# Optimization experiments

Measured on AMD Instinct MI355X. Metric: run time of the kernel, lower is better.

## Reference

```python
import jax, jax.numpy as jnp
import numpy as np

BS, T, NOBJ = 16, 32, 100
GLOVE, GEMB, ADIM, GCN_DIM, H, ASPACE, RES = 300, 64, 10, 512, 512, 6, 512


def setup_inputs() -> dict:
    key = jax.random.key(0)
    ks = jax.random.split(key, 34)
    rn = lambda k, shp, s=0.02: (jax.random.normal(k, shp, jnp.float32) * s)
    inp = {}
    inp["target"] = jax.random.normal(ks[0], (BS, T, GLOVE), jnp.float32)
    inp["input_"] = jax.random.normal(ks[1], (BS, T, RES, 1, 1), jnp.float32)
    inp["action_probs"] = jax.random.uniform(ks[2], (BS, T, ASPACE), jnp.float32)
    # symmetric normalized adjacency (D^-1/2 A D^-1/2), as normalize_adj produces
    A_raw = (jax.random.uniform(ks[3], (NOBJ, NOBJ)) < 0.1).astype(jnp.float32)
    A_raw = ((A_raw + A_raw.T + jnp.eye(NOBJ)) > 0).astype(jnp.float32)
    dinv = 1.0 / jnp.sqrt(jnp.sum(A_raw, axis=1))
    inp["A"] = A_raw * dinv[:, None] * dinv[None, :]
    inp["all_glove"] = jax.random.normal(ks[4], (NOBJ, GLOVE), jnp.float32)
    inp["Wword"] = rn(ks[5], (GEMB, GLOVE)); inp["bword"] = jnp.zeros((GEMB,))
    inp["Wg"] = rn(ks[6], (GEMB, GLOVE)); inp["bg"] = jnp.zeros((GEMB,))
    inp["Wa"] = rn(ks[7], (ADIM, ASPACE)); inp["ba"] = jnp.zeros((ADIM,))
    inp["W0"] = rn(ks[8], (256, RES + GEMB))
    inp["W1"] = rn(ks[9], (256, 256))
    inp["W2"] = rn(ks[10], (1, 256))
    inp["Wfm"] = rn(ks[11], (GCN_DIM, NOBJ)); inp["bfm"] = jnp.zeros((GCN_DIM,))
    fused_in = RES + GEMB + ADIM + GCN_DIM
    inp["Wf"] = rn(ks[12], (H, fused_in)); inp["bf"] = jnp.zeros((H,))
    inp["Wih"] = rn(ks[13], (4 * H, H)); inp["Whh"] = rn(ks[14], (4 * H, H))
    inp["bih"] = jnp.zeros((4 * H,)); inp["bhh"] = jnp.zeros((4 * H,))
    inp["Wa1"] = rn(ks[15], (128, H)); inp["ba1"] = jnp.zeros((128,))
    inp["Wa2"] = rn(ks[16], (ASPACE, 128)); inp["ba2"] = jnp.zeros((ASPACE,))
    inp["Wc1"] = rn(ks[17], (128, H)); inp["bc1"] = jnp.zeros((128,))
    inp["Wc2"] = rn(ks[18], (1, 128)); inp["bc2"] = jnp.zeros((1,))
    return inp


def _forward(target, input_, action_probs, A, all_glove, Wword, bword, Wg, bg,
             Wa, ba, W0, W1, W2, Wfm, bfm, Wf, bf, Wih, Whh, bih, bhh,
             Wa1, ba1, Wa2, ba2, Wc1, bc1, Wc2, bc2):
    bs, t = target.shape[0], target.shape[1]
    B = bs * t
    feats = input_.reshape(B, RES)                      # [B,512] (squeeze 1x1)
    glove_e = jax.nn.relu(target.reshape(B, GLOVE) @ Wg.T + bg)
    act_e = jax.nn.relu(action_probs.reshape(B, ASPACE) @ Wa.T + ba)
    # GCN branch (all_glove is detached in the original)
    word = jax.lax.stop_gradient(all_glove) @ Wword.T + bword   # [N,GEMB]
    N = A.shape[0]
    class_e = jnp.broadcast_to(feats[:, None, :], (B, N, RES))
    x = jnp.concatenate([class_e, jnp.broadcast_to(word[None], (B, N, GEMB))], -1)
    x = jax.nn.relu(jnp.einsum('nm,bmd->bnd', A, x) @ W0.T)     # [B,N,256]
    x = jax.nn.relu(jnp.einsum('nm,bmd->bnd', A, x) @ W1.T)     # [B,N,256]
    x = jax.nn.relu(jnp.einsum('nm,bmd->bnd', A, x) @ W2.T)     # [B,N,1]
    gcn_e = x[..., 0] @ Wfm.T + bfm                             # [B,GCN_DIM]
    fused = jnp.concatenate([feats, glove_e, act_e, gcn_e], -1)
    out = jax.nn.relu(fused @ Wf.T + bf).reshape(bs, t, H)
    # LSTM (torch gate order i,f,g,o), batch_first, zero init state
    h0 = jnp.zeros((bs, H), out.dtype)
    c0 = jnp.zeros((bs, H), out.dtype)
    def step(carry, xt):
        h, c = carry
        g = xt @ Wih.T + h @ Whh.T + bih + bhh
        i, f, gg, o = jnp.split(g, 4, axis=-1)
        c = jax.nn.sigmoid(f) * c + jax.nn.sigmoid(i) * jnp.tanh(gg)
        h = jax.nn.sigmoid(o) * jnp.tanh(c)
        return (h, c), h
    (hT, cT), hs = jax.lax.scan(step, (h0, c0), out.transpose(1, 0, 2))
    sf = hs.transpose(1, 0, 2).reshape(B, H)
    actor = jax.nn.relu(jax.nn.relu(sf @ Wa1.T + ba1) @ Wa2.T + ba2).reshape(bs, t, ASPACE)
    critic = jax.nn.relu(jax.nn.relu(sf @ Wc1.T + bc1) @ Wc2.T + bc2).reshape(bs, t, 1)
    return actor, critic, hT[None], cT[None]


def reference(target, input_, action_probs, A, all_glove, Wword, bword, Wg, bg,
              Wa, ba, W0, W1, W2, Wfm, bfm, Wf, bf, Wih, Whh, bih, bhh,
              Wa1, ba1, Wa2, ba2, Wc1, bc1, Wc2, bc2):
    return _forward(target, input_, action_probs, A, all_glove, Wword, bword,
                    Wg, bg, Wa, ba, W0, W1, W2, Wfm, bfm, Wf, bf, Wih, Whh,
                    bih, bhh, Wa1, ba1, Wa2, ba2, Wc1, bc1, Wc2, bc2)
```

## Files before the change

### kernel.cpp

```cpp
#include <hip/hip_runtime.h>
#include <cmath>

constexpr int BSZ = 16, T = 32, NOBJ = 100;
constexpr int GLOVE = 300, GEMB = 64, ADIM = 10, GCN_DIM = 512, Hh = 512, ASPACE = 6, RES = 512;
constexpr int Bt = BSZ * T;
constexpr int FUSED_IN = RES + GEMB + ADIM + GCN_DIM;
constexpr int FP = 1120;

typedef __attribute__((ext_vector_type(8))) short bf16x8;
typedef __attribute__((ext_vector_type(4))) float f32x4;

__device__ __forceinline__ unsigned short f2bf(float f) {
    unsigned u = __float_as_uint(f);
    return (unsigned short)((u + 0x7FFFu + ((u >> 16) & 1u)) >> 16);
}
__device__ __forceinline__ unsigned pk2(float a, float b) {
    return (unsigned)f2bf(a) | ((unsigned)f2bf(b) << 16);
}
__device__ __forceinline__ float sigf(float x) { return 1.f / (1.f + __expf(-x)); }

template<bool RELU, int OMODE>
__global__ __launch_bounds__(256)
void mgemm(const unsigned short* __restrict__ A, int lda,
           const unsigned short* __restrict__ B, int ldb,
           float* __restrict__ Cf, unsigned short* __restrict__ Cb, int ldc,
           const float* __restrict__ bias, int K)
{
    const int tid = threadIdx.x;
    const int l = tid & 63, wv = tid >> 6;
    const int m0 = blockIdx.y * 64 + wv * 16;
    const int n0 = blockIdx.x * 64;
    const int lr = l & 15, kg = l >> 4;
    const unsigned short* ap = A + (long)(m0 + lr) * lda + kg * 8;
    const unsigned short* bp = B + (long)(n0 + lr) * ldb + kg * 8;
    const int nk = K >> 5;
    f32x4 acc0 = (f32x4){0.f, 0.f, 0.f, 0.f};
    f32x4 acc1 = acc0, acc2 = acc0, acc3 = acc0;
    bf16x8 a_[4], b0_[4], b1_[4], b2_[4], b3_[4];
#pragma unroll
    for (int s = 0; s < 4; ++s) {
        if (s < nk) {
            int k = s * 32;
            a_[s]  = *(const bf16x8*)(ap + k);
            b0_[s] = *(const bf16x8*)(bp + k);
            b1_[s] = *(const bf16x8*)(bp + 16 * ldb + k);
            b2_[s] = *(const bf16x8*)(bp + 32 * ldb + k);
            b3_[s] = *(const bf16x8*)(bp + 48 * ldb + k);
        }
    }
    for (int i = 0; i < nk; i += 4) {
#pragma unroll
        for (int s = 0; s < 4; ++s) {
            if (i + s < nk) {
                acc0 = __builtin_amdgcn_mfma_f32_16x16x32_bf16(a_[s], b0_[s], acc0, 0, 0, 0);
                acc1 = __builtin_amdgcn_mfma_f32_16x16x32_bf16(a_[s], b1_[s], acc1, 0, 0, 0);
                acc2 = __builtin_amdgcn_mfma_f32_16x16x32_bf16(a_[s], b2_[s], acc2, 0, 0, 0);
                acc3 = __builtin_amdgcn_mfma_f32_16x16x32_bf16(a_[s], b3_[s], acc3, 0, 0, 0);
                if (i + s + 4 < nk) {
                    int k = (i + s + 4) * 32;
                    a_[s]  = *(const bf16x8*)(ap + k);
                    b0_[s] = *(const bf16x8*)(bp + k);
                    b1_[s] = *(const bf16x8*)(bp + 16 * ldb + k);
                    b2_[s] = *(const bf16x8*)(bp + 32 * ldb + k);
                    b3_[s] = *(const bf16x8*)(bp + 48 * ldb + k);
                }
            }
        }
    }
    f32x4 av[4] = {acc0, acc1, acc2, acc3};
#pragma unroll
    for (int nf = 0; nf < 4; ++nf) {
        int n = n0 + nf * 16 + lr;
        float bs = bias ? bias[n] : 0.f;
#pragma unroll
        for (int r = 0; r < 4; ++r) {
            float val = av[nf][r] + bs;
            if (RELU) val = fmaxf(val, 0.f);
            long idx = (long)(m0 + kg * 4 + r) * ldc + n;
            if (OMODE == 0) Cf[idx] = val;
            else            Cb[idx] = f2bf(val);
        }
    }
}

template<bool RELU>
__global__ __launch_bounds__(128)
void gemm32(const float* __restrict__ A, int lda,
            const float* __restrict__ B, int ldb,
            float* __restrict__ C, int ldc,
            const float* __restrict__ bias, int M, int N, int K)
{
    __shared__ float As[32][36];
    __shared__ float Bs[32][68];
    const int tid = threadIdx.x;
    const int m0 = blockIdx.y * 32, n0 = blockIdx.x * 64;
    const int mi = tid >> 4, ni = tid & 15;
    float acc[4][4] = {};
    for (int k0 = 0; k0 < K; k0 += 32) {
        __syncthreads();
#pragma unroll
        for (int l = 0; l < 2; ++l) {
            int e = tid + l * 128;
            int row = e >> 3, kq = (e & 7) << 2;
            float4 va = make_float4(0.f, 0.f, 0.f, 0.f);
            if (m0 + row < M && k0 + kq < K)
                va = *(const float4*)&A[(long)(m0 + row) * lda + k0 + kq];
            As[kq + 0][row] = va.x; As[kq + 1][row] = va.y;
            As[kq + 2][row] = va.z; As[kq + 3][row] = va.w;
        }
#pragma unroll
        for (int l = 0; l < 4; ++l) {
            int e = tid + l * 128;
            int row = e >> 3, kq = (e & 7) << 2;
            float4 vb = make_float4(0.f, 0.f, 0.f, 0.f);
            if (n0 + row < N && k0 + kq < K)
                vb = *(const float4*)&B[(long)(n0 + row) * ldb + k0 + kq];
            Bs[kq + 0][row] = vb.x; Bs[kq + 1][row] = vb.y;
            Bs[kq + 2][row] = vb.z; Bs[kq + 3][row] = vb.w;
        }
        __syncthreads();
#pragma unroll
        for (int k = 0; k < 32; ++k) {
            float4 a4 = *(const float4*)&As[k][4 * mi];
            float4 b4 = *(const float4*)&Bs[k][4 * ni];
            acc[0][0] = fmaf(a4.x, b4.x, acc[0][0]); acc[0][1] = fmaf(a4.x, b4.y, acc[0][1]);
            acc[0][2] = fmaf(a4.x, b4.z, acc[0][2]); acc[0][3] = fmaf(a4.x, b4.w, acc[0][3]);
            acc[1][0] = fmaf(a4.y, b4.x, acc[1][0]); acc[1][1] = fmaf(a4.y, b4.y, acc[1][1]);
            acc[1][2] = fmaf(a4.y, b4.z, acc[1][2]); acc[1][3] = fmaf(a4.y, b4.w, acc[1][3]);
            acc[2][0] = fmaf(a4.z, b4.x, acc[2][0]); acc[2][1] = fmaf(a4.z, b4.y, acc[2][1]);
            acc[2][2] = fmaf(a4.z, b4.z, acc[2][2]); acc[2][3] = fmaf(a4.z, b4.w, acc[2][3]);
            acc[3][0] = fmaf(a4.w, b4.x, acc[3][0]); acc[3][1] = fmaf(a4.w, b4.y, acc[3][1]);
            acc[3][2] = fmaf(a4.w, b4.z, acc[3][2]); acc[3][3] = fmaf(a4.w, b4.w, acc[3][3]);
        }
    }
    const int n = n0 + 4 * ni;
    if (n >= N) return;
    float4 bv = make_float4(0.f, 0.f, 0.f, 0.f);
    if (bias) bv = *(const float4*)&bias[n];
#pragma unroll
    for (int r = 0; r < 4; ++r) {
        int m = m0 + 4 * mi + r;
        if (m >= M) continue;
        float4 v;
        v.x = acc[r][0] + bv.x; v.y = acc[r][1] + bv.y;
        v.z = acc[r][2] + bv.z; v.w = acc[r][3] + bv.w;
        if (RELU) {
            v.x = fmaxf(v.x, 0.f); v.y = fmaxf(v.y, 0.f);
            v.z = fmaxf(v.z, 0.f); v.w = fmaxf(v.w, 0.f);
        }
        *(float4*)&C[(long)m * ldc + n] = v;
    }
}

__global__ __launch_bounds__(256)
void x1pack(const float* __restrict__ u, const float* __restrict__ v,
            const float* __restrict__ rowsum, uint4* __restrict__ X1g)
{
    __shared__ float u_lds[256];
    __shared__ float rs_lds[112];
    const int b = blockIdx.x, tid = threadIdx.x;
    u_lds[tid] = u[(long)b * 256 + tid];
    if (tid < 112) rs_lds[tid] = (tid < 100) ? rowsum[tid] : 0.f;
    __syncthreads();
    uint4* outp = X1g + (size_t)b * 3584;
#pragma unroll
    for (int it = 0; it < 14; ++it) {
        int job = it * 256 + tid;
        int l = job & 63;
        int kt = (job >> 6) & 7;
        int mt = job >> 9;
        int n = mt * 16 + (l & 15);
        int k0 = kt * 32 + ((l >> 4) << 3);
        uint4 p = make_uint4(0, 0, 0, 0);
        if (n < 100) {
            float rsn = rs_lds[n];
            float4 u0 = *(const float4*)&u_lds[k0];
            float4 u1 = *(const float4*)&u_lds[k0 + 4];
            const float4* vp = (const float4*)&v[n * 256 + k0];
            float4 v0 = vp[0], v1 = vp[1];
            float x0 = fmaxf(fmaf(rsn, u0.x, v0.x), 0.f), x1 = fmaxf(fmaf(rsn, u0.y, v0.y), 0.f);
            float x2 = fmaxf(fmaf(rsn, u0.z, v0.z), 0.f), x3 = fmaxf(fmaf(rsn, u0.w, v0.w), 0.f);
            float x4 = fmaxf(fmaf(rsn, u1.x, v1.x), 0.f), x5 = fmaxf(fmaf(rsn, u1.y, v1.y), 0.f);
            float x6 = fmaxf(fmaf(rsn, u1.z, v1.z), 0.f), x7 = fmaxf(fmaf(rsn, u1.w, v1.w), 0.f);
            p = make_uint4(pk2(x0, x1), pk2(x2, x3), pk2(x4, x5), pk2(x6, x7));
        }
        outp[job] = p;
    }
}

constexpr int ZLD = 152;

__global__ __launch_bounds__(256, 2)
void gcn_core(const bf16x8* __restrict__ X1g,
              const float* __restrict__ Aglob,
              const bf16x8* __restrict__ W1f,
              const bf16x8* __restrict__ Af,
              const float* __restrict__ w2,
              unsigned short* __restrict__ x3b)
{
    __shared__ unsigned short Z1Ts[128 * ZLD];
    __shared__ float w2l[256];
    __shared__ float spart[4][112];
    __shared__ float sl[112];

    const int b = blockIdx.x, tid = threadIdx.x;
    const int l = tid & 63, wv = tid >> 6;
    const int lrow = l & 15, kg = l >> 4;

    w2l[tid] = w2[tid];
    if (tid < 128) {
        uint4 z = make_uint4(0, 0, 0, 0);
        *(uint4*)&Z1Ts[tid * ZLD + 112] = z;
        *(uint4*)&Z1Ts[tid * ZLD + 120] = z;
    }
    if (tid < 28) x3b[(long)b * 128 + 100 + tid] = 0;
    __syncthreads();

    const bf16x8* xb = X1g + (size_t)b * 3584 + l;

    float sacc[7][4];
#pragma unroll
    for (int mt = 0; mt < 7; ++mt)
#pragma unroll
        for (int r = 0; r < 4; ++r) sacc[mt][r] = 0.f;

    for (int half = 0; half < 2; ++half) {
        f32x4 acc1[7][2];
#pragma unroll
        for (int mt = 0; mt < 7; ++mt)
#pragma unroll
            for (int jtl = 0; jtl < 2; ++jtl) acc1[mt][jtl] = (f32x4){0.f, 0.f, 0.f, 0.f};

#pragma unroll
        for (int kt = 0; kt < 8; ++kt) {
            bf16x8 af[7];
#pragma unroll
            for (int mt = 0; mt < 7; ++mt)
                af[mt] = xb[mt * 512 + kt * 64];
#pragma unroll
            for (int jtl = 0; jtl < 2; ++jtl) {
                int jt = half * 8 + wv * 2 + jtl;
                bf16x8 bfr = W1f[(jt * 8 + kt) * 64 + l];
#pragma unroll
                for (int mt = 0; mt < 7; ++mt)
                    acc1[mt][jtl] = __builtin_amdgcn_mfma_f32_16x16x32_bf16(af[mt], bfr, acc1[mt][jtl], 0, 0, 0);
            }
        }

#pragma unroll
        for (int mt = 0; mt < 7; ++mt)
#pragma unroll
            for (int jtl = 0; jtl < 2; ++jtl) {
                int jloc = (wv * 2 + jtl) * 16 + lrow;
                f32x4 a = acc1[mt][jtl];
                uint2 zz;
                zz.x = pk2(a[0], a[1]);
                zz.y = pk2(a[2], a[3]);
                *(uint2*)&Z1Ts[jloc * ZLD + mt * 16 + kg * 4] = zz;
            }

        bf16x8 bz[2][4];
#pragma unroll
        for (int jtl = 0; jtl < 2; ++jtl)
#pragma unroll
            for (int k2 = 0; k2 < 4; ++k2)
                bz[jtl][k2] = *(const bf16x8*)&Z1Ts[((wv * 2 + jtl) * 16 + lrow) * ZLD + k2 * 32 + kg * 8];
#pragma unroll
        for (int mt = 0; mt < 7; ++mt) {
            bf16x8 aA[4];
#pragma unroll
            for (int k2 = 0; k2 < 4; ++k2) aA[k2] = Af[(mt * 4 + k2) * 64 + l];
#pragma unroll
            for (int jtl = 0; jtl < 2; ++jtl) {
                f32x4 p = (f32x4){0.f, 0.f, 0.f, 0.f};
#pragma unroll
                for (int k2 = 0; k2 < 4; ++k2)
                    p = __builtin_amdgcn_mfma_f32_16x16x32_bf16(aA[k2], bz[jtl][k2], p, 0, 0, 0);
                float w2j = w2l[half * 128 + (wv * 2 + jtl) * 16 + lrow];
#pragma unroll
                for (int r = 0; r < 4; ++r)
                    sacc[mt][r] = fmaf(fmaxf(p[r], 0.f), w2j, sacc[mt][r]);
            }
        }
    }

#pragma unroll
    for (int mt = 0; mt < 7; ++mt) {
        float s0 = sacc[mt][0], s1 = sacc[mt][1], s2 = sacc[mt][2], s3 = sacc[mt][3];
#pragma unroll
        for (int off = 1; off < 16; off <<= 1) {
            s0 += __shfl_xor(s0, off);
            s1 += __shfl_xor(s1, off);
            s2 += __shfl_xor(s2, off);
            s3 += __shfl_xor(s3, off);
        }
        if (lrow == 0) {
            int m = mt * 16 + kg * 4;
            spart[wv][m + 0] = s0; spart[wv][m + 1] = s1;
            spart[wv][m + 2] = s2; spart[wv][m + 3] = s3;
        }
    }
    __syncthreads();
    if (tid < 112)
        sl[tid] = spart[0][tid] + spart[1][tid] + spart[2][tid] + spart[3][tid];
    __syncthreads();

    float sv0 = (l < 100) ? sl[l] : 0.f;
    float sv1 = (l + 64 < 100) ? sl[l + 64] : 0.f;
#pragma unroll 5
    for (int i = 0; i < 25; ++i) {
        int n = i * 4 + wv;
        float a0 = (l < 100) ? Aglob[n * 100 + l] : 0.f;
        float a1 = (l + 64 < 100) ? Aglob[n * 100 + l + 64] : 0.f;
        float p = a0 * sv0 + a1 * sv1;
#pragma unroll
        for (int off = 32; off; off >>= 1) p += __shfl_xor(p, off);
        if (l == 0) x3b[(long)b * 128 + n] = f2bf(fmaxf(p, 0.f));
    }
}

union HU { unsigned long long u[2]; bf16x8 v; };

__global__ __launch_bounds__(256)
void lstm_persist2(const float* __restrict__ xWih,
                   const bf16x8* __restrict__ Whhf,
                   unsigned long long* __restrict__ h0,
                   unsigned long long* __restrict__ h1,
                   float* __restrict__ cBuf, float* __restrict__ hFin,
                   unsigned short* __restrict__ sfb,
                   unsigned* __restrict__ bar)
{
    __shared__ float gl[4][16][17];
    __shared__ unsigned short htile[16][16];
    const int tid = threadIdx.x;
    const int l = tid & 63, g = tid >> 6;
    const int bid = blockIdx.x;
    const int jt = g * 32 + bid;
    const int lr = l & 15, kg = l >> 4;
    const bf16x8* wp = Whhf + (size_t)jt * 16 * 64 + l;
    bf16x8 w[16];
#pragma unroll
    for (int kt = 0; kt < 16; ++kt) w[kt] = wp[kt * 64];
    const int fb = tid >> 4, jl = tid & 15;
    const int jh = bid * 16 + jl;
    float c_reg = 0.f;
    unsigned long long* hprev = h0;
    unsigned long long* hnext = h1;
    for (int t = 0; t < T; ++t) {
        const unsigned long long* hp = hprev + lr * 128 + kg * 2;
        HU hu[16];
#pragma unroll
        for (int kt = 0; kt < 16; ++kt) {
            hu[kt].u[0] = __hip_atomic_load(hp + kt * 8,     __ATOMIC_RELAXED, __HIP_MEMORY_SCOPE_AGENT);
            hu[kt].u[1] = __hip_atomic_load(hp + kt * 8 + 1, __ATOMIC_RELAXED, __HIP_MEMORY_SCOPE_AGENT);
        }
        f32x4 acc = (f32x4){0.f, 0.f, 0.f, 0.f};
#pragma unroll
        for (int kt = 0; kt < 16; ++kt)
            acc = __builtin_amdgcn_mfma_f32_16x16x32_bf16(hu[kt].v, w[kt], acc, 0, 0, 0);
#pragma unroll
        for (int r = 0; r < 4; ++r) gl[g][kg * 4 + r][lr] = acc[r];
        __syncthreads();
        const float* xw = xWih + (size_t)(fb * T + t) * 2048;
        float gi = gl[0][fb][jl] + xw[jh];
        float gf = gl[1][fb][jl] + xw[512 + jh];
        float gg = gl[2][fb][jl] + xw[1024 + jh];
        float go = gl[3][fb][jl] + xw[1536 + jh];
        float cn = sigf(gf) * c_reg + sigf(gi) * tanhf(gg);
        float hn = sigf(go) * tanhf(cn);
        c_reg = cn;
        unsigned short hb = f2bf(hn);
        htile[fb][jl] = hb;
        sfb[(size_t)(fb * T + t) * 512 + jh] = hb;
        if (t == T - 1) { hFin[fb * 512 + jh] = hn; cBuf[fb * 512 + jh] = cn; }
        __syncthreads();
        if (tid < 64) {
            int row = tid >> 2, q = tid & 3;
            unsigned long long val = *(const unsigned long long*)&htile[row][q * 4];
            __hip_atomic_store(&hnext[row * 128 + bid * 4 + q], val,
                               __ATOMIC_RELAXED, __HIP_MEMORY_SCOPE_AGENT);
        }
        __syncthreads();
        if (tid == 0) {
            __hip_atomic_fetch_add(bar, 1u, __ATOMIC_RELAXED, __HIP_MEMORY_SCOPE_AGENT);
            unsigned tgt = 32u * (unsigned)(t + 1);
            while (__hip_atomic_load(bar, __ATOMIC_RELAXED, __HIP_MEMORY_SCOPE_AGENT) < tgt)
                __builtin_amdgcn_s_sleep(1);
        }
        __syncthreads();
        unsigned long long* tmp = hprev; hprev = hnext; hnext = tmp;
    }
}

__global__ void k_aw_rowsum(const float* __restrict__ A, const float* __restrict__ word,
                            float* __restrict__ Aw, float* __restrict__ rowsum)
{
    int i = blockIdx.x * 256 + threadIdx.x;
    if (i < 6400) {
        int n = i / 64, k = i % 64;
        float s = 0.f;
        for (int m = 0; m < 100; ++m) s += A[n * 100 + m] * word[m * 64 + k];
        Aw[i] = s;
    } else if (i < 6500) {
        int n = i - 6400;
        float s = 0.f;
        for (int m = 0; m < 100; ++m) s += A[n * 100 + m];
        rowsum[n] = s;
    }
}

__global__ void k_prep(const float* __restrict__ Whh, uint4* __restrict__ Whhf,
                       const float* __restrict__ Wf, unsigned short* __restrict__ WfPb,
                       const float* __restrict__ Wih, unsigned short* __restrict__ Wihb,
                       const float* __restrict__ Wa1, const float* __restrict__ Wc1,
                       unsigned short* __restrict__ Whdb,
                       const float* __restrict__ ba1, const float* __restrict__ bc1,
                       float* __restrict__ bhd,
                       const float* __restrict__ Wg, unsigned short* __restrict__ Wgb,
                       const float* __restrict__ W0, unsigned short* __restrict__ W0ab,
                       const float* __restrict__ Wfm, unsigned short* __restrict__ Wfmb,
                       const float* __restrict__ target, unsigned short* __restrict__ tgtb,
                       const float* __restrict__ feats, unsigned short* __restrict__ featsb,
                       unsigned short* __restrict__ fusedb,
                       const float* __restrict__ aprob, const float* __restrict__ Wa,
                       const float* __restrict__ ba,
                       unsigned short* __restrict__ hbA, unsigned* __restrict__ bar,
                       const float* __restrict__ bih, const float* __restrict__ bhh,
                       float* __restrict__ bsum,
                       const float* __restrict__ W1, uint4* __restrict__ W1f,
                       const float* __restrict__ A, uint4* __restrict__ Af)
{
    int bx = blockIdx.x, tid = threadIdx.x;
    if (bx < 512) {
        int job = bx * 256 + tid;
        int jtkt = job >> 6, ll = job & 63;
        int j = (jtkt >> 4) * 16 + (ll & 15);
        int k0 = (jtkt & 15) * 32 + (ll >> 4) * 8;
        const float* src = &Whh[(long)j * 512 + k0];
        uint4 p;
        p.x = pk2(src[0], src[1]); p.y = pk2(src[2], src[3]);
        p.z = pk2(src[4], src[5]); p.w = pk2(src[6], src[7]);
        Whhf[job] = p;
    } else if (bx < 2752) {
        int i = (bx - 512) * 256 + tid;
        int r = i / FP, c = i - r * FP;
        WfPb[i] = f2bf(c < FUSED_IN ? Wf[(long)r * FUSED_IN + c] : 0.f);
    } else if (bx < 6848) {
        int i = (bx - 2752) * 256 + tid;
        Wihb[i] = f2bf(Wih[i]);
    } else if (bx < 7360) {
        int i = (bx - 6848) * 256 + tid;
        int r = i >> 9, c = i & 511;
        Whdb[i] = f2bf(r < 128 ? Wa1[r * 512 + c] : Wc1[(r - 128) * 512 + c]);
    } else if (bx < 7361) {
        bhd[tid] = (tid < 128) ? ba1[tid] : bc1[tid - 128];
    } else if (bx < 7441) {
        int i = (bx - 7361) * 256 + tid;
        int r = i / 320, c = i - r * 320;
        Wgb[i] = f2bf(c < GLOVE ? Wg[r * GLOVE + c] : 0.f);
    } else if (bx < 7953) {
        int i = (bx - 7441) * 256 + tid;
        int r = i >> 9, c = i & 511;
        W0ab[i] = f2bf(W0[(long)r * 576 + c]);
    } else if (bx < 8209) {
        int i = (bx - 7953) * 256 + tid;
        int r = i >> 7, c = i & 127;
        Wfmb[i] = f2bf(c < 100 ? Wfm[r * 100 + c] : 0.f);
    } else if (bx < 8849) {
        int i = (bx - 8209) * 256 + tid;
        int r = i / 320, c = i - r * 320;
        tgtb[i] = f2bf(c < GLOVE ? target[(long)r * GLOVE + c] : 0.f);
    } else if (bx < 9873) {
        int i = (bx - 8849) * 256 + tid;
        featsb[i] = f2bf(feats[i]);
    } else if (bx < 10897) {
        int i = (bx - 9873) * 256 + tid;
        int r = i >> 9, c = i & 511;
        fusedb[(long)r * FP + c] = f2bf(feats[i]);
    } else if (bx < 10917) {
        int i = (bx - 10897) * 256 + tid;
        int r = i / 10, c6 = i - r * 10;
        float s = ba[c6];
#pragma unroll
        for (int k = 0; k < 6; ++k) s += aprob[r * 6 + k] * Wa[c6 * 6 + k];
        fusedb[(long)r * FP + 576 + c6] = f2bf(fmaxf(s, 0.f));
    } else if (bx < 10961) {
        int i = (bx - 10917) * 256 + tid;
        int r = i / 22, c = 1098 + (i - r * 22);
        fusedb[(long)r * FP + c] = 0;
    } else if (bx < 10993) {
        int i = (bx - 10961) * 256 + tid;
        hbA[i] = 0;
    } else if (bx < 10994) {
        if (tid == 0) bar[0] = 0u;
    } else if (bx < 11002) {
        int i = (bx - 10994) * 256 + tid;
        bsum[i] = bih[i] + bhh[i];
    } else if (bx < 11034) {
        int job = (bx - 11002) * 256 + tid;
        int jt = job >> 9, rem = job & 511, kt = rem >> 6, lane = rem & 63;
        int j = jt * 16 + (lane & 15), k0 = kt * 32 + (lane >> 4) * 8;
        const float* src = &W1[(long)j * 256 + k0];
        uint4 p;
        p.x = pk2(src[0], src[1]); p.y = pk2(src[2], src[3]);
        p.z = pk2(src[4], src[5]); p.w = pk2(src[6], src[7]);
        W1f[job] = p;
    } else {
        int job = (bx - 11034) * 256 + tid;
        int mt = job >> 8, rem = job & 255, kt = rem >> 6, lane = rem & 63;
        int m = mt * 16 + (lane & 15), n0 = kt * 32 + (lane >> 4) * 8;
        float h[8];
#pragma unroll
        for (int e = 0; e < 8; ++e)
            h[e] = (m < 100 && n0 + e < 100) ? A[m * 100 + n0 + e] : 0.f;
        uint4 p;
        p.x = pk2(h[0], h[1]); p.y = pk2(h[2], h[3]);
        p.z = pk2(h[4], h[5]); p.w = pk2(h[6], h[7]);
        Af[job] = p;
    }
}

__global__ void k_finish(const float* __restrict__ hd,
                         const float* __restrict__ Wa2, const float* __restrict__ ba2,
                         const float* __restrict__ Wc2, const float* __restrict__ bc2,
                         const float* __restrict__ hFin, const float* __restrict__ cBuf,
                         float* __restrict__ out)
{
    if (blockIdx.x < 32) {
        int row = blockIdx.x * 16 + (threadIdx.x >> 4);
        int slot = threadIdx.x & 15;
        if (slot < 6) {
            const float4* h4 = (const float4*)(hd + (long)row * 256);
            const float4* w4 = (const float4*)(Wa2 + slot * 128);
            float s = 0.f;
#pragma unroll
            for (int k = 0; k < 32; ++k) {
                float4 h = h4[k], w = w4[k];
                s += h.x * w.x + h.y * w.y + h.z * w.z + h.w * w.w;
            }
            out[row * 6 + slot] = fmaxf(s + ba2[slot], 0.f);
        } else if (slot == 6) {
            const float4* h4 = (const float4*)(hd + (long)row * 256 + 128);
            const float4* w4 = (const float4*)(Wc2);
            float s = 0.f;
#pragma unroll
            for (int k = 0; k < 32; ++k) {
                float4 h = h4[k], w = w4[k];
                s += h.x * w.x + h.y * w.y + h.z * w.z + h.w * w.w;
            }
            out[3072 + row] = fmaxf(s + bc2[0], 0.f);
        }
    } else {
        int i = (blockIdx.x - 32) * 256 + threadIdx.x;
        out[3584 + i] = hFin[i];
        out[11776 + i] = cBuf[i];
    }
}

static inline void mg(hipStream_t st, const unsigned short* A, int lda,
                      const unsigned short* B, int ldb,
                      float* Cf, unsigned short* Cb, int ldc,
                      const float* bias, int M, int N, int K, bool relu, bool bf16out)
{
    dim3 g(N / 64, M / 64), blk(256);
    if (bf16out) {
        if (relu) hipLaunchKernelGGL((mgemm<true, 1>), g, blk, 0, st, A, lda, B, ldb, Cf, Cb, ldc, bias, K);
        else      hipLaunchKernelGGL((mgemm<false, 1>), g, blk, 0, st, A, lda, B, ldb, Cf, Cb, ldc, bias, K);
    } else {
        if (relu) hipLaunchKernelGGL((mgemm<true, 0>), g, blk, 0, st, A, lda, B, ldb, Cf, Cb, ldc, bias, K);
        else      hipLaunchKernelGGL((mgemm<false, 0>), g, blk, 0, st, A, lda, B, ldb, Cf, Cb, ldc, bias, K);
    }
}
static inline void g32(hipStream_t st, const float* A, int lda, const float* B, int ldb,
                       float* C, int ldc, const float* bias, int M, int N, int K, bool relu)
{
    dim3 g((N + 63) / 64, (M + 31) / 32), blk(128);
    if (relu) hipLaunchKernelGGL((gemm32<true>), g, blk, 0, st, A, lda, B, ldb, C, ldc, bias, M, N, K);
    else      hipLaunchKernelGGL((gemm32<false>), g, blk, 0, st, A, lda, B, ldb, C, ldc, bias, M, N, K);
}

extern "C" void kernel_launch(void* const* d_in, const int* in_sizes, int n_in,
                              void* d_out, int out_size, void* d_ws, size_t ws_size,
                              hipStream_t stream)
{
    const float* target = (const float*)d_in[0];
    const float* input_ = (const float*)d_in[1];
    const float* aprob  = (const float*)d_in[2];
    const float* Adj    = (const float*)d_in[3];
    const float* aglove = (const float*)d_in[4];
    const float* Wword  = (const float*)d_in[5];
    const float* bword  = (const float*)d_in[6];
    const float* Wg     = (const float*)d_in[7];
    const float* bg     = (const float*)d_in[8];
    const float* Wa     = (const float*)d_in[9];
    const float* ba     = (const float*)d_in[10];
    const float* W0     = (const float*)d_in[11];
    const float* W1     = (const float*)d_in[12];
    const float* W2     = (const float*)d_in[13];
    const float* Wfm    = (const float*)d_in[14];
    const float* bfm    = (const float*)d_in[15];
    const float* Wf     = (const float*)d_in[16];
    const float* bf     = (const float*)d_in[17];
    const float* Wih    = (const float*)d_in[18];
    const float* Whh    = (const float*)d_in[19];
    const float* bih    = (const float*)d_in[20];
    const float* bhh    = (const float*)d_in[21];
    const float* Wa1    = (const float*)d_in[22];
    const float* ba1    = (const float*)d_in[23];
    const float* Wa2    = (const float*)d_in[24];
    const float* ba2    = (const float*)d_in[25];
    const float* Wc1    = (const float*)d_in[26];
    const float* bc1    = (const float*)d_in[27];
    const float* Wc2    = (const float*)d_in[28];
    const float* bc2    = (const float*)d_in[29];

    float* ws = (float*)d_ws;
    float* out = (float*)d_out;

    size_t off = 0;
    auto alloc = [&](size_t n) { size_t r = off; off += (n + 255) & ~(size_t)255; return r; };
    float* u       = ws + alloc(512 * 256);
    float* word    = ws + alloc(100 * 64);
    float* Aw      = ws + alloc(100 * 64);
    float* rowsum  = ws + alloc(128);
    float* v       = ws + alloc(100 * 256);
    float* bsum    = ws + alloc(2048);
    float* bhd     = ws + alloc(256);
    float* xWih    = ws + alloc((size_t)512 * 2048);
    float* hd      = ws + alloc(512 * 256);
    float* hFin    = ws + alloc(BSZ * Hh);
    float* cBuf    = ws + alloc(BSZ * Hh);
    float* W1frag  = ws + alloc(32768);
    float* Afrag   = ws + alloc(7168);
    float* Whhf    = ws + alloc((size_t)524288);
    float* X1gf    = ws + alloc((size_t)512 * 3584 * 4);
    unsigned* bar  = (unsigned*)(ws + alloc(256));
    unsigned short* x3b     = (unsigned short*)(ws + alloc(512 * 128 / 2));
    unsigned short* fusedb  = (unsigned short*)(ws + alloc((size_t)512 * FP / 2));
    unsigned short* WfPb    = (unsigned short*)(ws + alloc((size_t)512 * FP / 2));
    unsigned short* outfb   = (unsigned short*)(ws + alloc(512 * 512 / 2));
    unsigned short* Wihb    = (unsigned short*)(ws + alloc((size_t)2048 * 512 / 2));
    unsigned short* Whdb    = (unsigned short*)(ws + alloc(256 * 512 / 2));
    unsigned short* Wgb     = (unsigned short*)(ws + alloc(64 * 320 / 2));
    unsigned short* W0ab    = (unsigned short*)(ws + alloc(256 * 512 / 2));
    unsigned short* Wfmb    = (unsigned short*)(ws + alloc(512 * 128 / 2));
    unsigned short* tgtb    = (unsigned short*)(ws + alloc(512 * 320 / 2));
    unsigned short* featsb  = (unsigned short*)(ws + alloc(512 * 512 / 2));
    unsigned short* sfb     = (unsigned short*)(ws + alloc(512 * 512 / 2));
    unsigned short* hbA     = (unsigned short*)(ws + alloc(BSZ * Hh / 2));
    unsigned short* hbB     = (unsigned short*)(ws + alloc(BSZ * Hh / 2));
    (void)ws_size; (void)in_sizes; (void)n_in; (void)out_size;

    const float* feats = input_;

    hipLaunchKernelGGL(k_prep, dim3(11041), dim3(256), 0, stream,
                       Whh, (uint4*)Whhf, Wf, WfPb, Wih, Wihb, Wa1, Wc1, Whdb, ba1, bc1, bhd,
                       Wg, Wgb, W0, W0ab, Wfm, Wfmb, target, tgtb, feats, featsb,
                       fusedb, aprob, Wa, ba, hbA, bar, bih, bhh, bsum,
                       W1, (uint4*)W1frag, Adj, (uint4*)Afrag);

    g32(stream, aglove, GLOVE, Wword, GLOVE, word, 64, bword, 100, 64, GLOVE, false);
    hipLaunchKernelGGL(k_aw_rowsum, dim3(26), dim3(256), 0, stream, Adj, word, Aw, rowsum);
    g32(stream, Aw, 64, W0 + 512, 576, v, 256, nullptr, 100, 256, 64, false);

    mg(stream, featsb, 512, W0ab, 512, u, nullptr, 256, nullptr, 512, 256, 512, false, false);
    mg(stream, tgtb, 320, Wgb, 320, nullptr, fusedb + 512, FP, bg, 512, 64, 320, true, true);

    hipLaunchKernelGGL(x1pack, dim3(Bt), dim3(256), 0, stream, u, v, rowsum, (uint4*)X1gf);
    hipLaunchKernelGGL(gcn_core, dim3(Bt), dim3(256), 0, stream,
                       (const bf16x8*)X1gf, Adj, (const bf16x8*)W1frag, (const bf16x8*)Afrag, W2, x3b);
    mg(stream, x3b, 128, Wfmb, 128, nullptr, fusedb + 586, FP, bfm, 512, 512, 128, false, true);

    mg(stream, fusedb, FP, WfPb, FP, nullptr, outfb, 512, bf, 512, 512, FP, true, true);
    mg(stream, outfb, 512, Wihb, 512, xWih, nullptr, 2048, bsum, 512, 2048, 512, false, false);

    hipLaunchKernelGGL(lstm_persist2, dim3(32), dim3(256), 0, stream,
                       xWih, (const bf16x8*)Whhf,
                       (unsigned long long*)hbA, (unsigned long long*)hbB,
                       cBuf, hFin, sfb, bar);

    mg(stream, sfb, 512, Whdb, 512, hd, nullptr, 256, bhd, 512, 256, 512, true, false);
    hipLaunchKernelGGL(k_finish, dim3(64), dim3(256), 0, stream,
                       hd, Wa2, ba2, Wc2, bc2, hFin, cBuf, out);
}
```

Before: 375.5 us.

## Replace LSTM grid barrier with per-step flag array and time-indexed h buffers

After: 377.0 us. Within noise of the previous version (+0.4%).

```diff
diff --git a/kernel.cpp b/kernel.cpp
--- a/kernel.cpp
+++ b/kernel.cpp
@@ -321,14 +321,13 @@
 
 union HU { unsigned long long u[2]; bf16x8 v; };
 
-__global__ __launch_bounds__(256)
-void lstm_persist2(const float* __restrict__ xWih,
+__global__ __launch_bounds__(256, 1)
+void lstm_persist3(const float* __restrict__ xWih,
                    const bf16x8* __restrict__ Whhf,
-                   unsigned long long* __restrict__ h0,
-                   unsigned long long* __restrict__ h1,
+                   unsigned long long* __restrict__ hseq,
+                   unsigned* __restrict__ flags,
                    float* __restrict__ cBuf, float* __restrict__ hFin,
-                   unsigned short* __restrict__ sfb,
-                   unsigned* __restrict__ bar)
+                   unsigned short* __restrict__ sfb)
 {
     __shared__ float gl[4][16][17];
     __shared__ unsigned short htile[16][16];
@@ -344,10 +343,15 @@
     const int fb = tid >> 4, jl = tid & 15;
     const int jh = bid * 16 + jl;
     float c_reg = 0.f;
-    unsigned long long* hprev = h0;
-    unsigned long long* hnext = h1;
     for (int t = 0; t < T; ++t) {
-        const unsigned long long* hp = hprev + lr * 128 + kg * 2;
+        if (t > 0) {
+            if (tid < 32) {
+                while (__hip_atomic_load(&flags[t * 32 + tid],
+                                         __ATOMIC_RELAXED, __HIP_MEMORY_SCOPE_AGENT) == 0u) { }
+            }
+            __syncthreads();
+        }
+        const unsigned long long* hp = hseq + (size_t)t * 2048 + lr * 128 + kg * 2;
         HU hu[16];
 #pragma unroll
         for (int kt = 0; kt < 16; ++kt) {
@@ -377,18 +381,13 @@
         if (tid < 64) {
             int row = tid >> 2, q = tid & 3;
             unsigned long long val = *(const unsigned long long*)&htile[row][q * 4];
-            __hip_atomic_store(&hnext[row * 128 + bid * 4 + q], val,
+            __hip_atomic_store(&hseq[(size_t)(t + 1) * 2048 + row * 128 + bid * 4 + q], val,
                                __ATOMIC_RELAXED, __HIP_MEMORY_SCOPE_AGENT);
         }
         __syncthreads();
-        if (tid == 0) {
-            __hip_atomic_fetch_add(bar, 1u, __ATOMIC_RELAXED, __HIP_MEMORY_SCOPE_AGENT);
-            unsigned tgt = 32u * (unsigned)(t + 1);
-            while (__hip_atomic_load(bar, __ATOMIC_RELAXED, __HIP_MEMORY_SCOPE_AGENT) < tgt)
-                __builtin_amdgcn_s_sleep(1);
-        }
-        __syncthreads();
-        unsigned long long* tmp = hprev; hprev = hnext; hnext = tmp;
+        if (tid == 0)
+            __hip_atomic_store(&flags[(t + 1) * 32 + bid], 1u,
+                               __ATOMIC_RELAXED, __HIP_MEMORY_SCOPE_AGENT);
     }
 }
 
@@ -424,7 +423,7 @@
                        unsigned short* __restrict__ fusedb,
                        const float* __restrict__ aprob, const float* __restrict__ Wa,
                        const float* __restrict__ ba,
-                       unsigned short* __restrict__ hbA, unsigned* __restrict__ bar,
+                       unsigned short* __restrict__ h0s, unsigned* __restrict__ flags,
                        const float* __restrict__ bih, const float* __restrict__ bhh,
                        float* __restrict__ bsum,
                        const float* __restrict__ W1, uint4* __restrict__ W1f,
@@ -490,14 +489,15 @@
         fusedb[(long)r * FP + c] = 0;
     } else if (bx < 10993) {
         int i = (bx - 10961) * 256 + tid;
-        hbA[i] = 0;
-    } else if (bx < 10994) {
-        if (tid == 0) bar[0] = 0u;
-    } else if (bx < 11002) {
-        int i = (bx - 10994) * 256 + tid;
+        h0s[i] = 0;
+    } else if (bx < 10998) {
+        int i = (bx - 10993) * 256 + tid;
+        if (i < (T + 1) * 32) flags[i] = 0u;
+    } else if (bx < 11006) {
+        int i = (bx - 10998) * 256 + tid;
         bsum[i] = bih[i] + bhh[i];
-    } else if (bx < 11034) {
-        int job = (bx - 11002) * 256 + tid;
+    } else if (bx < 11038) {
+        int job = (bx - 11006) * 256 + tid;
         int jt = job >> 9, rem = job & 511, kt = rem >> 6, lane = rem & 63;
         int j = jt * 16 + (lane & 15), k0 = kt * 32 + (lane >> 4) * 8;
         const float* src = &W1[(long)j * 256 + k0];
@@ -506,7 +506,7 @@
         p.z = pk2(src[4], src[5]); p.w = pk2(src[6], src[7]);
         W1f[job] = p;
     } else {
-        int job = (bx - 11034) * 256 + tid;
+        int job = (bx - 11038) * 256 + tid;
         int mt = job >> 8, rem = job & 255, kt = rem >> 6, lane = rem & 63;
         int m = mt * 16 + (lane & 15), n0 = kt * 32 + (lane >> 4) * 8;
         float h[8];
@@ -634,7 +634,8 @@
     float* Afrag   = ws + alloc(7168);
     float* Whhf    = ws + alloc((size_t)524288);
     float* X1gf    = ws + alloc((size_t)512 * 3584 * 4);
-    unsigned* bar  = (unsigned*)(ws + alloc(256));
+    float* hseqf   = ws + alloc((size_t)(T + 1) * 2048 * 2);
+    unsigned* flags = (unsigned*)(ws + alloc(2048));
     unsigned short* x3b     = (unsigned short*)(ws + alloc(512 * 128 / 2));
     unsigned short* fusedb  = (unsigned short*)(ws + alloc((size_t)512 * FP / 2));
     unsigned short* WfPb    = (unsigned short*)(ws + alloc((size_t)512 * FP / 2));
@@ -647,16 +648,15 @@
     unsigned short* tgtb    = (unsigned short*)(ws + alloc(512 * 320 / 2));
     unsigned short* featsb  = (unsigned short*)(ws + alloc(512 * 512 / 2));
     unsigned short* sfb     = (unsigned short*)(ws + alloc(512 * 512 / 2));
-    unsigned short* hbA     = (unsigned short*)(ws + alloc(BSZ * Hh / 2));
-    unsigned short* hbB     = (unsigned short*)(ws + alloc(BSZ * Hh / 2));
     (void)ws_size; (void)in_sizes; (void)n_in; (void)out_size;
 
     const float* feats = input_;
 
-    hipLaunchKernelGGL(k_prep, dim3(11041), dim3(256), 0, stream,
+    hipLaunchKernelGGL(k_prep, dim3(11045), dim3(256), 0, stream,
                        Whh, (uint4*)Whhf, Wf, WfPb, Wih, Wihb, Wa1, Wc1, Whdb, ba1, bc1, bhd,
                        Wg, Wgb, W0, W0ab, Wfm, Wfmb, target, tgtb, feats, featsb,
-                       fusedb, aprob, Wa, ba, hbA, bar, bih, bhh, bsum,
+                       fusedb, aprob, Wa, ba,
+                       (unsigned short*)hseqf, flags, bih, bhh, bsum,
                        W1, (uint4*)W1frag, Adj, (uint4*)Afrag);
 
     g32(stream, aglove, GLOVE, Wword, GLOVE, word, 64, bword, 100, 64, GLOVE, false);
@@ -674,10 +674,9 @@
     mg(stream, fusedb, FP, WfPb, FP, nullptr, outfb, 512, bf, 512, 512, FP, true, true);
     mg(stream, outfb, 512, Wihb, 512, xWih, nullptr, 2048, bsum, 512, 2048, 512, false, false);
 
-    hipLaunchKernelGGL(lstm_persist2, dim3(32), dim3(256), 0, stream,
+    hipLaunchKernelGGL(lstm_persist3, dim3(32), dim3(256), 0, stream,
                        xWih, (const bf16x8*)Whhf,
-                       (unsigned long long*)hbA, (unsigned long long*)hbB,
-                       cBuf, hFin, sfb, bar);
+                       (unsigned long long*)hseqf, flags, cBuf, hFin, sfb);
 
     mg(stream, sfb, 512, Whdb, 512, hd, nullptr, 256, bhd, 512, 256, 512, true, false);
     hipLaunchKernelGGL(k_finish, dim3(64), dim3(256), 0, stream,
```
